# Kernel optimization log

Hardware: AMD Instinct MI355X
Metric: run time of the kernel (lower is better)

## Reference

```python
import jax, jax.numpy as jnp
import numpy as np

B, S, E, H, DH, F = 4, 2048, 1024, 4, 256, 4096


def setup_inputs() -> dict:
    key = jax.random.key(0)
    ks = jax.random.split(key, 16)
    def w(k, shape):
        return jax.random.normal(k, shape, jnp.float32) * 0.02
    return {
        "inputs": jax.random.normal(ks[0], (B, S, E), jnp.float32),
        "context": jax.random.normal(ks[1], (B, S, E), jnp.float32),
        # self-attention (causal) per-head projections stacked over heads
        "Wk1": w(ks[2], (H, E, DH)), "bk1": jnp.zeros((H, DH), jnp.float32),
        "Wq1": w(ks[3], (H, E, DH)), "bq1": jnp.zeros((H, DH), jnp.float32),
        "Wv1": w(ks[4], (H, E, DH)), "bv1": jnp.zeros((H, DH), jnp.float32),
        "Wo1": w(ks[5], (E, E)), "bo1": jnp.zeros((E,), jnp.float32),
        # cross-attention (no mask)
        "Wk2": w(ks[6], (H, E, DH)), "bk2": jnp.zeros((H, DH), jnp.float32),
        "Wq2": w(ks[7], (H, E, DH)), "bq2": jnp.zeros((H, DH), jnp.float32),
        "Wv2": w(ks[8], (H, E, DH)), "bv2": jnp.zeros((H, DH), jnp.float32),
        "Wo2": w(ks[9], (E, E)), "bo2": jnp.zeros((E,), jnp.float32),
        "ln_g": jnp.ones((E,), jnp.float32), "ln_b": jnp.zeros((E,), jnp.float32),
        # FFN
        "W1": w(ks[10], (E, F)), "b1": jnp.zeros((F,), jnp.float32),
        "W2": w(ks[11], (F, E)), "b2": jnp.zeros((E,), jnp.float32),
    }


def _mha(kin, vin, qin, Wk, bk, Wq, bq, Wv, bv, Wo, bo, causal):
    # per-head Dense projections, batched over heads: [B,S,E] x [H,E,DH] -> [B,H,S,DH]
    K = jnp.einsum('bse,hed->bhsd', kin, Wk) + bk[None, :, None, :]
    Q = jnp.einsum('bse,hed->bhsd', qin, Wq) + bq[None, :, None, :]
    V = jnp.einsum('bse,hed->bhsd', vin, Wv) + bv[None, :, None, :]
    # NOTE: original divides by head_dim (K.get_shape()[2]), NOT sqrt(head_dim)
    scores = jnp.einsum('bhqd,bhkd->bhqk', Q, K) / K.shape[-1]
    if causal:
        sq, sk = scores.shape[-2], scores.shape[-1]
        mask = jnp.triu(jnp.full((sq, sk), -jnp.inf, scores.dtype), k=1)
        scores = scores + mask  # additive -inf strictly above the diagonal
    A = jax.nn.softmax(scores, axis=-1)
    # concat heads in order along the feature axis, then output Dense
    out = jnp.einsum('bhqk,bhkd->bqhd', A, V).reshape(qin.shape[0], qin.shape[1], -1)
    return out @ Wo + bo


def _ln(x, g, b):
    # keras LayerNormalization default epsilon = 1e-3
    m = x.mean(-1, keepdims=True)
    v = ((x - m) ** 2).mean(-1, keepdims=True)
    return (x - m) / jnp.sqrt(v + 1e-3) * g + b


def reference(inputs, context, Wk1, bk1, Wq1, bq1, Wv1, bv1, Wo1, bo1,
              Wk2, bk2, Wq2, bq2, Wv2, bv2, Wo2, bo2,
              ln_g, ln_b, W1, b1, W2, b2):
    # dropout layers are identity at inference
    a = _mha(inputs, inputs, inputs, Wk1, bk1, Wq1, bq1, Wv1, bv1, Wo1, bo1, True) + inputs
    a = _ln(a, ln_g, ln_b)
    # cross-attention: keys/values = context, queries = normalized self-attn output
    c = _mha(context, context, a, Wk2, bk2, Wq2, bq2, Wv2, bv2, Wo2, bo2, False) + a
    c = _ln(c, ln_g, ln_b)
    h = jax.nn.relu(c @ W1 + b1) @ W2 + b2 + c
    return jax.nn.relu(_ln(h, ln_g, ln_b))
```

## Files before the change

kernel.cpp:

```cpp
#include <hip/hip_runtime.h>

#define DEV __device__ __forceinline__

typedef unsigned short u16;
typedef __bf16 bf16x8 __attribute__((ext_vector_type(8)));
typedef bf16x8 __attribute__((may_alias)) bf16x8a;
typedef float f32x4 __attribute__((ext_vector_type(4)));
typedef float f32x16 __attribute__((ext_vector_type(16)));

constexpr int NB = 4, NS = 2048, NE = 1024, NH = 4, NDH = 256, NF = 4096;
constexpr int NR = NB * NS;

DEV u16 f2bf(float f) {
  unsigned u = __float_as_uint(f);
  u += 0x7fff + ((u >> 16) & 1);
  return (u16)(u >> 16);
}

DEV f32x4 mfma16(bf16x8 a, bf16x8 b, f32x4 c) {
  return __builtin_amdgcn_mfma_f32_16x16x32_bf16(a, b, c, 0, 0, 0);
}
DEV f32x16 mfma32(bf16x8 a, bf16x8 b, f32x16 c) {
  return __builtin_amdgcn_mfma_f32_32x32x16_bf16(a, b, c, 0, 0, 0);
}

DEV bf16x8 ldfrag(const u16* p) { return *(const bf16x8a*)p; }

DEV void gload_lds16(const void* g, void* l) {
  __builtin_amdgcn_global_load_lds(
      (const __attribute__((address_space(1))) void*)g,
      (__attribute__((address_space(3))) void*)l, 16, 0, 0);
}

DEV void blockbar() {
  asm volatile("" ::: "memory");
  __builtin_amdgcn_s_barrier();
  asm volatile("" ::: "memory");
}

DEV unsigned packbf(float a, float b) {
  union { __bf16 h[2]; unsigned u; } x;
  x.h[0] = (__bf16)a; x.h[1] = (__bf16)b;
  return x.u;
}

__global__ void cast_f32_bf16(const float* __restrict__ in, u16* __restrict__ out, int n4) {
  int i = blockIdx.x * 256 + threadIdx.x;
  if (i >= n4) return;
  float4 v = ((const float4*)in)[i];
  ushort4 o;
  o.x = f2bf(v.x); o.y = f2bf(v.y); o.z = f2bf(v.z); o.w = f2bf(v.w);
  ((ushort4*)out)[i] = o;
}

__global__ void transpose_cast(const float* __restrict__ in, u16* __restrict__ out, int R, int C) {
  __shared__ float t[32][33];
  size_t base = (size_t)blockIdx.z * R * C;
  int c0 = blockIdx.x * 32, r0 = blockIdx.y * 32;
  int x = threadIdx.x;
  for (int yy = threadIdx.y; yy < 32; yy += 8)
    t[yy][x] = in[base + (size_t)(r0 + yy) * C + c0 + x];
  __syncthreads();
  for (int yy = threadIdx.y; yy < 32; yy += 8)
    out[base + (size_t)(c0 + yy) * R + r0 + x] = f2bf(t[x][yy]);
}

__global__ void transpose_v(const u16* __restrict__ V, int vstride, u16* __restrict__ Vt) {
  __shared__ u16 t[32][34];
  int bh = blockIdx.z, b = bh >> 2, h = bh & (NH - 1);
  int s0 = blockIdx.x * 32, d0 = blockIdx.y * 32;
  int x = threadIdx.x;
  for (int yy = threadIdx.y; yy < 32; yy += 8)
    t[yy][x] = V[(size_t)(b * NS + s0 + yy) * vstride + h * NDH + d0 + x];
  __syncthreads();
  for (int yy = threadIdx.y; yy < 32; yy += 8)
    Vt[((size_t)bh * NDH + d0 + yy) * NS + s0 + x] = t[x][yy];
}

__global__ void copy_f32(const float* __restrict__ s, float* __restrict__ d, int n) {
  int i = blockIdx.x * 256 + threadIdx.x;
  if (i < n) d[i] = s[i];
}

template<int OUTF32, int RELU>
__global__ __launch_bounds__(256, 2)
void gemm_bt(const u16* __restrict__ A, const u16* __restrict__ Bt,
             const float* __restrict__ bias, const float* __restrict__ res,
             float* __restrict__ outF, u16* __restrict__ outB,
             int M, int N, int K)
{
  __shared__ u16 lA[128 * 32];
  __shared__ u16 lB[128 * 32];
  int tid = threadIdx.x;
  int wid = tid >> 6, lane = tid & 63;
  int lr = lane & 15, lk = lane >> 4;
  int wm = wid >> 1, wn = wid & 1;

  int flat = blockIdx.y * gridDim.x + blockIdx.x;
  int cpx = (gridDim.x * gridDim.y) >> 3;
  int swz = (flat & 7) * cpx + (flat >> 3);
  int bx = swz % gridDim.x, by = swz / gridDim.x;
  int rowBlk = by * 128, colBlk = bx * 128;

  f32x4 acc[4][4];
#pragma unroll
  for (int i = 0; i < 4; i++)
#pragma unroll
    for (int j = 0; j < 4; j++) acc[i][j] = (f32x4){0.f, 0.f, 0.f, 0.f};

  const u16* gA = A + (size_t)(rowBlk + wid * 32 + (lane >> 2)) * K + (lane & 3) * 8;
  const u16* gB = Bt + (size_t)(colBlk + wid * 32 + (lane >> 2)) * K + (lane & 3) * 8;
  u16* lAw = lA + wid * 1024;
  u16* lBw = lB + wid * 1024;

  for (int kk = 0; kk < K; kk += 32) {
    __syncthreads();
    gload_lds16(gA + kk, lAw);
    gload_lds16(gA + kk + (size_t)16 * K, lAw + 512);
    gload_lds16(gB + kk, lBw);
    gload_lds16(gB + kk + (size_t)16 * K, lBw + 512);
    asm volatile("s_waitcnt vmcnt(0)" ::: "memory");
    __syncthreads();

    bf16x8 af[4], bf[4];
#pragma unroll
    for (int fm = 0; fm < 4; fm++)
      af[fm] = ldfrag(lA + (wm * 64 + fm * 16 + lr) * 32 + lk * 8);
#pragma unroll
    for (int fn = 0; fn < 4; fn++)
      bf[fn] = ldfrag(lB + (wn * 64 + fn * 16 + lr) * 32 + lk * 8);
#pragma unroll
    for (int fm = 0; fm < 4; fm++)
#pragma unroll
      for (int fn = 0; fn < 4; fn++)
        acc[fm][fn] = mfma16(af[fm], bf[fn], acc[fm][fn]);
  }

  int orow = rowBlk + wm * 64;
  int ocol = colBlk + wn * 64;
#pragma unroll
  for (int fn = 0; fn < 4; fn++) {
    int c = ocol + fn * 16 + lr;
    float bv = bias[c];
#pragma unroll
    for (int fm = 0; fm < 4; fm++) {
      int r0 = orow + fm * 16 + lk * 4;
#pragma unroll
      for (int j = 0; j < 4; j++) {
        float v = acc[fm][fn][j] + bv;
        if (OUTF32) v += res[(size_t)(r0 + j) * N + c];
        if (RELU) v = fmaxf(v, 0.f);
        if (OUTF32) outF[(size_t)(r0 + j) * N + c] = v;
        else        outB[(size_t)(r0 + j) * N + c] = f2bf(v);
      }
    }
  }
}

template<int CAUSAL>
__global__ __launch_bounds__(256, 1)
void attn32(const u16* __restrict__ Qp, int qstride,
            const u16* __restrict__ Kp, int kstride,
            const u16* __restrict__ Vt, u16* __restrict__ O)
{
  int bidx = blockIdx.x;
  int bh = bidx & 15;
  int qt = CAUSAL ? (15 - (bidx >> 4)) : (bidx >> 4);
  int b = bh >> 2, h = bh & 3;
  int tid = threadIdx.x, wid = tid >> 6, lane = tid & 63;
  int L = lane & 31, hi = lane >> 5;

  __shared__ __align__(16) u16 lK[2][8192];
  __shared__ __align__(16) u16 lV[2][8192];

  const u16* qrow = Qp + (size_t)(b * NS + qt * 128 + wid * 32 + L) * qstride + h * NDH;
  bf16x8 qf[16];
#pragma unroll
  for (int s = 0; s < 16; s++) qf[s] = ldfrag(qrow + s * 16 + hi * 8);

  f32x16 oacc[8];
#pragma unroll
  for (int db = 0; db < 8; db++) oacc[db] = (f32x16){};
  float m = -1e30f, l = 0.f;

  int nkt = CAUSAL ? (4 * qt + 4) : (NS / 32);
  int kdiag = 4 * qt + wid;
  constexpr float SC = 1.0f / NDH;

  const u16* kbase = Kp + (size_t)(b * NS) * kstride + h * NDH;
  const u16* vbase = Vt + (size_t)bh * NDH * NS;

  auto stage = [&](int kt, int buf) {
#pragma unroll
    for (int ii = 0; ii < 4; ii++) {
      int gi = wid * 4 + ii;
      int krow = 2 * gi + hi;
      int kcol = L ^ krow;
      gload_lds16(kbase + (size_t)(kt * 32 + krow) * kstride + kcol * 8,
                  &lK[buf][gi * 512]);
      int vd = 16 * gi + (lane >> 2);
      int vc = (lane & 3) ^ (vd & 3);
      gload_lds16(vbase + (size_t)vd * NS + kt * 32 + vc * 8,
                  &lV[buf][gi * 512]);
    }
  };

  stage(0, 0);

  for (int kt = 0; kt < nkt; kt++) {
    int buf = kt & 1;
    if (kt + 1 < nkt) {
      stage(kt + 1, buf ^ 1);
      asm volatile("s_waitcnt vmcnt(8)" ::: "memory");
    } else {
      asm volatile("s_waitcnt vmcnt(0)" ::: "memory");
    }
    blockbar();

    if (!CAUSAL || kt <= kdiag) {
      f32x16 sa = (f32x16){};
#pragma unroll
      for (int s = 0; s < 16; s++) {
        bf16x8 kf = ldfrag(&lK[buf][L * 256 + (((2 * s + hi) ^ L) & 31) * 8]);
        sa = mfma32(kf, qf[s], sa);
      }

      float p[16];
      float tmax = -1e30f;
#pragma unroll
      for (int r = 0; r < 16; r++) {
        float v = sa[r] * SC;
        if (CAUSAL) {
          if (kt == kdiag) {
            int key = (r & 3) + 8 * (r >> 2) + 4 * hi;
            if (kt * 32 + key > qt * 128 + wid * 32 + L) v = -1e30f;
          }
        }
        p[r] = v;
        tmax = fmaxf(tmax, v);
      }
      tmax = fmaxf(tmax, __shfl_xor(tmax, 32));

      float mn = m;
      if (!__all(tmax - m <= 5.0f)) {
        mn = fmaxf(m, tmax);
        float rs = __expf(m - mn);
        m = mn;
        l *= rs;
#pragma unroll
        for (int db = 0; db < 8; db++)
#pragma unroll
          for (int r = 0; r < 16; r++) oacc[db][r] *= rs;
      }
      float psum = 0.f;
#pragma unroll
      for (int r = 0; r < 16; r++) {
        p[r] = __expf(p[r] - mn);
        psum += p[r];
      }
      psum += __shfl_xor(psum, 32);
      l += psum;

      unsigned pk01 = packbf(p[0], p[1]),  pk23 = packbf(p[2], p[3]);
      unsigned pk45 = packbf(p[4], p[5]),  pk67 = packbf(p[6], p[7]);
      unsigned pk89 = packbf(p[8], p[9]),  pkab = packbf(p[10], p[11]);
      unsigned pkcd = packbf(p[12], p[13]), pkef = packbf(p[14], p[15]);
      unsigned s45 = (unsigned)__shfl_xor((int)pk45, 32);
      unsigned s67 = (unsigned)__shfl_xor((int)pk67, 32);
      unsigned s01 = (unsigned)__shfl_xor((int)pk01, 32);
      unsigned s23 = (unsigned)__shfl_xor((int)pk23, 32);
      unsigned scd = (unsigned)__shfl_xor((int)pkcd, 32);
      unsigned sef = (unsigned)__shfl_xor((int)pkef, 32);
      unsigned s89 = (unsigned)__shfl_xor((int)pk89, 32);
      unsigned sab = (unsigned)__shfl_xor((int)pkab, 32);
      union { unsigned u[4]; bf16x8 v; } fb0, fb1;
      fb0.u[0] = hi ? s45 : pk01;
      fb0.u[1] = hi ? s67 : pk23;
      fb0.u[2] = hi ? pk45 : s01;
      fb0.u[3] = hi ? pk67 : s23;
      fb1.u[0] = hi ? scd : pk89;
      fb1.u[1] = hi ? sef : pkab;
      fb1.u[2] = hi ? pkcd : s89;
      fb1.u[3] = hi ? pkef : sab;
      bf16x8 pb0 = fb0.v, pb1 = fb1.v;

#pragma unroll
      for (int db = 0; db < 8; db++) {
        int d = db * 32 + L;
        bf16x8 vf0 = ldfrag(&lV[buf][d * 32 + ((hi ^ (d & 3)) & 3) * 8]);
        bf16x8 vf1 = ldfrag(&lV[buf][d * 32 + (((2 + hi) ^ (d & 3)) & 3) * 8]);
        oacc[db] = mfma32(vf0, pb0, oacc[db]);
        oacc[db] = mfma32(vf1, pb1, oacc[db]);
      }
    }
    blockbar();
  }

  float inv = 1.f / l;
  size_t orow = (size_t)(b * NS + qt * 128 + wid * 32 + L) * NE + h * NDH;
#pragma unroll
  for (int db = 0; db < 8; db++) {
#pragma unroll
    for (int rq = 0; rq < 4; rq++) {
      float a0 = oacc[db][rq * 4 + 0] * inv, a1 = oacc[db][rq * 4 + 1] * inv;
      float a2 = oacc[db][rq * 4 + 2] * inv, a3 = oacc[db][rq * 4 + 3] * inv;
      uint2 w;
      w.x = packbf(a0, a1);
      w.y = packbf(a2, a3);
      *(uint2*)&O[orow + db * 32 + rq * 8 + hi * 4] = w;
    }
  }
}

template<int RELU, int WBF>
__global__ __launch_bounds__(256)
void ln_kernel(const float* __restrict__ x, const float* __restrict__ g,
               const float* __restrict__ bb, float* __restrict__ outF,
               u16* __restrict__ outB)
{
  int row = blockIdx.x, tid = threadIdx.x;
  float4 v = ((const float4*)(x + (size_t)row * NE))[tid];
  float s = v.x + v.y + v.z + v.w;
  float s2 = v.x * v.x + v.y * v.y + v.z * v.z + v.w * v.w;
#pragma unroll
  for (int off = 32; off; off >>= 1) {
    s += __shfl_xor(s, off);
    s2 += __shfl_xor(s2, off);
  }
  __shared__ float red[8];
  int wid = tid >> 6, lane = tid & 63;
  if (lane == 0) { red[wid] = s; red[4 + wid] = s2; }
  __syncthreads();
  s = red[0] + red[1] + red[2] + red[3];
  s2 = red[4] + red[5] + red[6] + red[7];
  float mean = s * (1.f / NE);
  float var = s2 * (1.f / NE) - mean * mean;
  float rstd = rsqrtf(var + 1e-3f);
  float4 gg = ((const float4*)g)[tid];
  float4 bv = ((const float4*)bb)[tid];
  float4 o;
  o.x = (v.x - mean) * rstd * gg.x + bv.x;
  o.y = (v.y - mean) * rstd * gg.y + bv.y;
  o.z = (v.z - mean) * rstd * gg.z + bv.z;
  o.w = (v.w - mean) * rstd * gg.w + bv.w;
  if (RELU) {
    o.x = fmaxf(o.x, 0.f); o.y = fmaxf(o.y, 0.f);
    o.z = fmaxf(o.z, 0.f); o.w = fmaxf(o.w, 0.f);
  }
  ((float4*)(outF + (size_t)row * NE))[tid] = o;
  if (WBF) {
    ushort4 ob;
    ob.x = f2bf(o.x); ob.y = f2bf(o.y); ob.z = f2bf(o.z); ob.w = f2bf(o.w);
    ((ushort4*)(outB + (size_t)row * NE))[tid] = ob;
  }
}

constexpr size_t OFF_X    = 0;
constexpr size_t OFF_W    = OFF_X + 16777216;
constexpr size_t OFF_BIAS = OFF_W + 33554432;
constexpr size_t OFF_QKV  = OFF_BIAS + 32768;
constexpr size_t OFF_VT   = OFF_QKV + 50331648;
constexpr size_t OFF_T0   = OFF_VT + 16777216;
constexpr size_t OFF_A    = OFF_T0 + 33554432;
constexpr size_t OFF_ABF  = OFF_A + 33554432;

extern "C" void kernel_launch(void* const* d_in, const int* in_sizes, int n_in,
                              void* d_out, int out_size, void* d_ws, size_t ws_size,
                              hipStream_t stream) {
  (void)in_sizes; (void)n_in; (void)out_size; (void)ws_size;
  const float* inp = (const float*)d_in[0];
  const float* ctx = (const float*)d_in[1];
  const float* Wk1 = (const float*)d_in[2];  const float* bk1 = (const float*)d_in[3];
  const float* Wq1 = (const float*)d_in[4];  const float* bq1 = (const float*)d_in[5];
  const float* Wv1 = (const float*)d_in[6];  const float* bv1 = (const float*)d_in[7];
  const float* Wo1 = (const float*)d_in[8];  const float* bo1 = (const float*)d_in[9];
  const float* Wk2 = (const float*)d_in[10]; const float* bk2 = (const float*)d_in[11];
  const float* Wq2 = (const float*)d_in[12]; const float* bq2 = (const float*)d_in[13];
  const float* Wv2 = (const float*)d_in[14]; const float* bv2 = (const float*)d_in[15];
  const float* Wo2 = (const float*)d_in[16]; const float* bo2 = (const float*)d_in[17];
  const float* lng = (const float*)d_in[18]; const float* lnb = (const float*)d_in[19];
  const float* W1  = (const float*)d_in[20]; const float* b1  = (const float*)d_in[21];
  const float* W2  = (const float*)d_in[22]; const float* b2  = (const float*)d_in[23];
  float* out = (float*)d_out;
  char* ws = (char*)d_ws;

  u16* XBF    = (u16*)(ws + OFF_X);
  u16* WQKV1T = (u16*)(ws + OFF_W);
  u16* WKV2T  = WQKV1T + 3072 * 1024;
  u16* WQ2T   = WKV2T + 2048 * 1024;
  u16* WO1T   = WQ2T + 1024 * 1024;
  u16* WO2T   = WO1T + 1024 * 1024;
  u16* W1T    = WO2T + 1024 * 1024;
  u16* W2T    = W1T + 4096 * 1024;
  float* BQKV1 = (float*)(ws + OFF_BIAS);
  float* BKV2  = BQKV1 + 3072;
  u16* QKV  = (u16*)(ws + OFF_QKV);
  u16* Q2   = QKV + 8192 * 2048;
  u16* VT   = (u16*)(ws + OFF_VT);
  u16* MID  = QKV;
  float* T0 = (float*)(ws + OFF_T0);
  float* Af = (float*)(ws + OFF_A);
  u16* ABF  = (u16*)(ws + OFF_ABF);
  u16* Obuf = XBF;

  dim3 tb(32, 8);

  cast_f32_bf16<<<8192, 256, 0, stream>>>(inp, XBF, NR * NE / 4);
  transpose_cast<<<dim3(8, 32, 4), tb, 0, stream>>>(Wk1, WQKV1T,               NE, NDH);
  transpose_cast<<<dim3(8, 32, 4), tb, 0, stream>>>(Wq1, WQKV1T + 1024 * 1024, NE, NDH);
  transpose_cast<<<dim3(8, 32, 4), tb, 0, stream>>>(Wv1, WQKV1T + 2048 * 1024, NE, NDH);
  transpose_cast<<<dim3(32, 32, 1), tb, 0, stream>>>(Wo1, WO1T, NE, NE);
  transpose_cast<<<dim3(8, 32, 4), tb, 0, stream>>>(Wk2, WKV2T,               NE, NDH);
  transpose_cast<<<dim3(8, 32, 4), tb, 0, stream>>>(Wv2, WKV2T + 1024 * 1024, NE, NDH);
  transpose_cast<<<dim3(8, 32, 4), tb, 0, stream>>>(Wq2, WQ2T, NE, NDH);
  transpose_cast<<<dim3(32, 32, 1), tb, 0, stream>>>(Wo2, WO2T, NE, NE);
  transpose_cast<<<dim3(128, 32, 1), tb, 0, stream>>>(W1, W1T, NE, NF);
  transpose_cast<<<dim3(32, 128, 1), tb, 0, stream>>>(W2, W2T, NF, NE);
  copy_f32<<<4, 256, 0, stream>>>(bk1, BQKV1, 1024);
  copy_f32<<<4, 256, 0, stream>>>(bq1, BQKV1 + 1024, 1024);
  copy_f32<<<4, 256, 0, stream>>>(bv1, BQKV1 + 2048, 1024);
  copy_f32<<<4, 256, 0, stream>>>(bk2, BKV2, 1024);
  copy_f32<<<4, 256, 0, stream>>>(bv2, BKV2 + 1024, 1024);

  gemm_bt<0, 0><<<dim3(24, 64), 256, 0, stream>>>(XBF, WQKV1T, BQKV1, nullptr,
                                                  nullptr, QKV, NR, 3072, NE);
  transpose_v<<<dim3(64, 8, 16), tb, 0, stream>>>(QKV + 2048, 3072, VT);
  attn32<1><<<256, 256, 0, stream>>>(QKV + 1024, 3072, QKV, 3072, VT, Obuf);
  gemm_bt<1, 0><<<dim3(8, 64), 256, 0, stream>>>(Obuf, WO1T, bo1, inp,
                                                 T0, nullptr, NR, NE, NE);
  ln_kernel<0, 1><<<NR, 256, 0, stream>>>(T0, lng, lnb, Af, ABF);

  cast_f32_bf16<<<8192, 256, 0, stream>>>(ctx, XBF, NR * NE / 4);
  gemm_bt<0, 0><<<dim3(16, 64), 256, 0, stream>>>(XBF, WKV2T, BKV2, nullptr,
                                                  nullptr, QKV, NR, 2048, NE);
  gemm_bt<0, 0><<<dim3(8, 64), 256, 0, stream>>>(ABF, WQ2T, bq2, nullptr,
                                                 nullptr, Q2, NR, NE, NE);
  transpose_v<<<dim3(64, 8, 16), tb, 0, stream>>>(QKV + 1024, 2048, VT);
  attn32<0><<<256, 256, 0, stream>>>(Q2, 1024, QKV, 2048, VT, Obuf);
  gemm_bt<1, 0><<<dim3(8, 64), 256, 0, stream>>>(Obuf, WO2T, bo2, Af,
                                                 T0, nullptr, NR, NE, NE);
  ln_kernel<0, 1><<<NR, 256, 0, stream>>>(T0, lng, lnb, Af, ABF);

  gemm_bt<0, 1><<<dim3(32, 64), 256, 0, stream>>>(ABF, W1T, b1, nullptr,
                                                  nullptr, MID, NR, NF, NE);
  gemm_bt<1, 0><<<dim3(8, 64), 256, 0, stream>>>(MID, W2T, b2, Af,
                                                 T0, nullptr, NR, NE, NF);
  ln_kernel<1, 0><<<NR, 256, 0, stream>>>(T0, lng, lnb, out, nullptr);
}
```

Baseline: 822.4 us.

## Split attention key range across wave pairs with LDS merge of partial softmax

The attention kernel now runs 8 waves per block, with each pair of waves sharing a 32-row query group and each wave handling half of a 64-key tile. Partial max, sum and output accumulators are merged through LDS at the end. This doubles the waves available to hide latency and halves the serial key-loop length per block. It also adds s_setprio around the MFMA sections. The cost is a 128KB LDS footprint, extra barriers and a final reduction pass.

```diff
diff --git a/kernel.cpp b/kernel.cpp
--- a/kernel.cpp
+++ b/kernel.cpp
@@ -158,22 +158,24 @@
 }
 
 template<int CAUSAL>
-__global__ __launch_bounds__(256, 1)
-void attn32(const u16* __restrict__ Qp, int qstride,
+__global__ __launch_bounds__(512, 2)
+void attn8w(const u16* __restrict__ Qp, int qstride,
             const u16* __restrict__ Kp, int kstride,
             const u16* __restrict__ Vt, u16* __restrict__ O)
 {
+  __shared__ __align__(16) u16 smem[65536];
+
   int bidx = blockIdx.x;
   int bh = bidx & 15;
   int qt = CAUSAL ? (15 - (bidx >> 4)) : (bidx >> 4);
   int b = bh >> 2, h = bh & 3;
-  int tid = threadIdx.x, wid = tid >> 6, lane = tid & 63;
+  int tid = threadIdx.x, w = tid >> 6, lane = tid & 63;
   int L = lane & 31, hi = lane >> 5;
-
-  __shared__ __align__(16) u16 lK[2][8192];
-  __shared__ __align__(16) u16 lV[2][8192];
-
-  const u16* qrow = Qp + (size_t)(b * NS + qt * 128 + wid * 32 + L) * qstride + h * NDH;
+  int g = w >> 1, ks = w & 1;
+
+  int qbase = qt * 128 + g * 32;
+
+  const u16* qrow = Qp + (size_t)(b * NS + qbase + L) * qstride + h * NDH;
   bf16x8 qf[16];
 #pragma unroll
   for (int s = 0; s < 16; s++) qf[s] = ldfrag(qrow + s * 16 + hi * 8);
@@ -183,8 +185,7 @@
   for (int db = 0; db < 8; db++) oacc[db] = (f32x16){};
   float m = -1e30f, l = 0.f;
 
-  int nkt = CAUSAL ? (4 * qt + 4) : (NS / 32);
-  int kdiag = 4 * qt + wid;
+  int nkt = CAUSAL ? (2 * qt + 2) : (NS / 64);
   constexpr float SC = 1.0f / NDH;
 
   const u16* kbase = Kp + (size_t)(b * NS) * kstride + h * NDH;
@@ -193,15 +194,15 @@
   auto stage = [&](int kt, int buf) {
 #pragma unroll
     for (int ii = 0; ii < 4; ii++) {
-      int gi = wid * 4 + ii;
+      int gi = w * 4 + ii;
       int krow = 2 * gi + hi;
-      int kcol = L ^ krow;
-      gload_lds16(kbase + (size_t)(kt * 32 + krow) * kstride + kcol * 8,
-                  &lK[buf][gi * 512]);
-      int vd = 16 * gi + (lane >> 2);
-      int vc = (lane & 3) ^ (vd & 3);
-      gload_lds16(vbase + (size_t)vd * NS + kt * 32 + vc * 8,
-                  &lV[buf][gi * 512]);
+      int kcol = L ^ (krow & 31);
+      gload_lds16(kbase + (size_t)(kt * 64 + krow) * kstride + kcol * 8,
+                  &smem[buf * 16384 + gi * 512]);
+      int vd = gi * 8 + (lane >> 3);
+      int vg = (lane & 7) ^ (vd & 7);
+      gload_lds16(vbase + (size_t)vd * NS + kt * 64 + vg * 8,
+                  &smem[32768 + buf * 16384 + gi * 512]);
     }
   };
 
@@ -209,6 +210,8 @@
 
   for (int kt = 0; kt < nkt; kt++) {
     int buf = kt & 1;
+    const u16* bK = &smem[buf * 16384];
+    const u16* bV = &smem[32768 + buf * 16384];
     if (kt + 1 < nkt) {
       stage(kt + 1, buf ^ 1);
       asm volatile("s_waitcnt vmcnt(8)" ::: "memory");
@@ -217,24 +220,28 @@
     }
     blockbar();
 
-    if (!CAUSAL || kt <= kdiag) {
+    int ksub0 = kt * 64 + ks * 32;
+    bool skip = CAUSAL && (ksub0 > qbase + 31);
+    if (!skip) {
+      bool domask = CAUSAL && (ksub0 + 31 > qbase);
+      __builtin_amdgcn_s_setprio(1);
       f32x16 sa = (f32x16){};
 #pragma unroll
       for (int s = 0; s < 16; s++) {
-        bf16x8 kf = ldfrag(&lK[buf][L * 256 + (((2 * s + hi) ^ L) & 31) * 8]);
+        int row = ks * 32 + L;
+        bf16x8 kf = ldfrag(&bK[row * 256 + (((2 * s + hi) ^ L) & 31) * 8]);
         sa = mfma32(kf, qf[s], sa);
       }
+      __builtin_amdgcn_s_setprio(0);
 
       float p[16];
       float tmax = -1e30f;
 #pragma unroll
       for (int r = 0; r < 16; r++) {
         float v = sa[r] * SC;
-        if (CAUSAL) {
-          if (kt == kdiag) {
-            int key = (r & 3) + 8 * (r >> 2) + 4 * hi;
-            if (kt * 32 + key > qt * 128 + wid * 32 + L) v = -1e30f;
-          }
+        if (domask) {
+          int key = ksub0 + (r & 3) + 8 * (r >> 2) + 4 * hi;
+          if (key > qbase + L) v = -1e30f;
         }
         p[r] = v;
         tmax = fmaxf(tmax, v);
@@ -284,30 +291,58 @@
       fb1.u[3] = hi ? pkef : sab;
       bf16x8 pb0 = fb0.v, pb1 = fb1.v;
 
+      __builtin_amdgcn_s_setprio(1);
 #pragma unroll
       for (int db = 0; db < 8; db++) {
-        int d = db * 32 + L;
-        bf16x8 vf0 = ldfrag(&lV[buf][d * 32 + ((hi ^ (d & 3)) & 3) * 8]);
-        bf16x8 vf1 = ldfrag(&lV[buf][d * 32 + (((2 + hi) ^ (d & 3)) & 3) * 8]);
+        int vd = db * 32 + L;
+        bf16x8 vf0 = ldfrag(&bV[vd * 64 + (((ks * 4 + hi) ^ (vd & 7)) & 7) * 8]);
+        bf16x8 vf1 = ldfrag(&bV[vd * 64 + (((ks * 4 + 2 + hi) ^ (vd & 7)) & 7) * 8]);
         oacc[db] = mfma32(vf0, pb0, oacc[db]);
         oacc[db] = mfma32(vf1, pb1, oacc[db]);
       }
+      __builtin_amdgcn_s_setprio(0);
     }
     blockbar();
   }
 
-  float inv = 1.f / l;
-  size_t orow = (size_t)(b * NS + qt * 128 + wid * 32 + L) * NE + h * NDH;
-#pragma unroll
-  for (int db = 0; db < 8; db++) {
-#pragma unroll
-    for (int rq = 0; rq < 4; rq++) {
-      float a0 = oacc[db][rq * 4 + 0] * inv, a1 = oacc[db][rq * 4 + 1] * inv;
-      float a2 = oacc[db][rq * 4 + 2] * inv, a3 = oacc[db][rq * 4 + 3] * inv;
-      uint2 w;
-      w.x = packbf(a0, a1);
-      w.y = packbf(a2, a3);
-      *(uint2*)&O[orow + db * 32 + rq * 8 + hi * 4] = w;
+  float* fsm = (float*)smem;
+  blockbar();
+  if (hi == 0) { fsm[w * 64 + L * 2] = m; fsm[w * 64 + L * 2 + 1] = l; }
+  blockbar();
+  float mb = fsm[(w ^ 1) * 64 + L * 2];
+  float lb = fsm[(w ^ 1) * 64 + L * 2 + 1];
+  float M = fmaxf(m, mb);
+  float eo = __expf(m - M);
+  float lt = l * eo + lb * __expf(mb - M);
+  blockbar();
+  float* reg = fsm + g * 8192;
+  if (w & 1) {
+#pragma unroll
+    for (int db = 0; db < 8; db++)
+#pragma unroll
+      for (int r = 0; r < 16; r++) {
+        int d = db * 32 + (r & 3) + 8 * (r >> 2) + 4 * hi;
+        reg[d * 32 + L] = oacc[db][r] * eo;
+      }
+  }
+  blockbar();
+  if (!(w & 1)) {
+    float inv = 1.f / lt;
+    size_t orow = (size_t)(b * NS + qbase + L) * NE + h * NDH;
+#pragma unroll
+    for (int db = 0; db < 8; db++) {
+#pragma unroll
+      for (int rq = 0; rq < 4; rq++) {
+        int d0 = db * 32 + rq * 8 + hi * 4;
+        float a0 = (oacc[db][rq * 4 + 0] * eo + reg[(d0 + 0) * 32 + L]) * inv;
+        float a1 = (oacc[db][rq * 4 + 1] * eo + reg[(d0 + 1) * 32 + L]) * inv;
+        float a2 = (oacc[db][rq * 4 + 2] * eo + reg[(d0 + 2) * 32 + L]) * inv;
+        float a3 = (oacc[db][rq * 4 + 3] * eo + reg[(d0 + 3) * 32 + L]) * inv;
+        uint2 wv;
+        wv.x = packbf(a0, a1);
+        wv.y = packbf(a2, a3);
+        *(uint2*)&O[orow + d0] = wv;
+      }
     }
   }
 }
@@ -425,7 +460,7 @@
   gemm_bt<0, 0><<<dim3(24, 64), 256, 0, stream>>>(XBF, WQKV1T, BQKV1, nullptr,
                                                   nullptr, QKV, NR, 3072, NE);
   transpose_v<<<dim3(64, 8, 16), tb, 0, stream>>>(QKV + 2048, 3072, VT);
-  attn32<1><<<256, 256, 0, stream>>>(QKV + 1024, 3072, QKV, 3072, VT, Obuf);
+  attn8w<1><<<256, 512, 0, stream>>>(QKV + 1024, 3072, QKV, 3072, VT, Obuf);
   gemm_bt<1, 0><<<dim3(8, 64), 256, 0, stream>>>(Obuf, WO1T, bo1, inp,
                                                  T0, nullptr, NR, NE, NE);
   ln_kernel<0, 1><<<NR, 256, 0, stream>>>(T0, lng, lnb, Af, ABF);
@@ -436,7 +471,7 @@
   gemm_bt<0, 0><<<dim3(8, 64), 256, 0, stream>>>(ABF, WQ2T, bq2, nullptr,
                                                  nullptr, Q2, NR, NE, NE);
   transpose_v<<<dim3(64, 8, 16), tb, 0, stream>>>(QKV + 1024, 2048, VT);
-  attn32<0><<<256, 256, 0, stream>>>(Q2, 1024, QKV, 2048, VT, Obuf);
+  attn8w<0><<<256, 512, 0, stream>>>(Q2, 1024, QKV, 2048, VT, Obuf);
   gemm_bt<1, 0><<<dim3(8, 64), 256, 0, stream>>>(Obuf, WO2T, bo2, Af,
                                                  T0, nullptr, NR, NE, NE);
   ln_kernel<0, 1><<<NR, 256, 0, stream>>>(T0, lng, lnb, Af, ABF);
```

New measurement: 789.1 us. 1.04x faster.
